# Performance work log

Measured on AMD Instinct MI355X. Metric: run time of the kernel, lower is better.

The kernel has to match this reference:

```python
import jax, jax.numpy as jnp
import numpy as np

NUM_EXPERTS = 16
HIDDEN = 2048
INTERMEDIATE = 1408
TOTAL_TOKENS = 32768  # tokens pre-sorted by expert assignment


def setup_inputs() -> dict:
    key = jax.random.key(0)
    k1, k2, k3, k4 = jax.random.split(key, 4)
    x = jax.random.normal(k1, (TOTAL_TOKENS, HIDDEN), dtype=jnp.float32)
    # normal() initializer per module; scale ~N(0, 0.02) like typical kernel_init
    w_gate = jax.random.normal(k2, (NUM_EXPERTS, HIDDEN, INTERMEDIATE), dtype=jnp.float32) * 0.02
    w_up = jax.random.normal(k3, (NUM_EXPERTS, HIDDEN, INTERMEDIATE), dtype=jnp.float32) * 0.02
    w_down = jax.random.normal(k4, (NUM_EXPERTS, INTERMEDIATE, HIDDEN), dtype=jnp.float32) * 0.02
    # tokens evenly distributed over experts; sums to TOTAL_TOKENS
    group_sizes = jnp.full((NUM_EXPERTS,), TOTAL_TOKENS // NUM_EXPERTS, dtype=jnp.int32)
    return {"x": x, "w_gate": w_gate, "w_up": w_up, "w_down": w_down,
            "group_sizes": group_sizes}


def reference(x, w_gate, w_up, w_down, group_sizes):
    # Grouped (ragged) GEMMs: rows of x are grouped contiguously by expert,
    # group_sizes[e] rows use expert e's kernel. lax.ragged_dot is the
    # idiomatic grouped-GEMM primitive (no dense [T,E] masking).
    gate = jax.lax.ragged_dot(x, w_gate, group_sizes)      # [T, I]
    up = jax.lax.ragged_dot(x, w_up, group_sizes)          # [T, I]
    h = jax.nn.silu(gate) * up                             # fused SwiGLU gating
    out = jax.lax.ragged_dot(h, w_down, group_sizes)       # [T, H]
    return out
```

## Files before the change

kernel.cpp:

```cpp
#include <hip/hip_runtime.h>
#include <hip/hip_bf16.h>

#define TOKENS 32768
#define NEXP   16
#define HID    2048
#define IMD    1408
#define BM 256
#define BK 64

typedef __bf16 bf16x8 __attribute__((ext_vector_type(8)));
typedef float  f32x4  __attribute__((ext_vector_type(4)));
typedef unsigned short u16x8 __attribute__((ext_vector_type(8)));

using gptr1_t = const __attribute__((address_space(1))) void*;
using lptr3_t = __attribute__((address_space(3))) void*;

static __device__ __forceinline__ unsigned short f2bf(float f) {
  unsigned int x = __builtin_bit_cast(unsigned int, f);
  x += 0x7fffu + ((x >> 16) & 1u);
  return (unsigned short)(x >> 16);
}
static __device__ __forceinline__ float bf2f(unsigned short u) {
  unsigned int x = ((unsigned int)u) << 16;
  return __builtin_bit_cast(float, x);
}
static __device__ __forceinline__ void gload16(const void* g, void* l) {
  __builtin_amdgcn_global_load_lds((gptr1_t)g, (lptr3_t)l, 16, 0, 0);
}
static __device__ __forceinline__ void vwait(int n) {
  switch (n) {
    case 0:  asm volatile("s_waitcnt vmcnt(0)" ::: "memory"); break;
    case 2:  asm volatile("s_waitcnt vmcnt(2)" ::: "memory"); break;
    default: asm volatile("s_waitcnt vmcnt(6)" ::: "memory"); break;
  }
}

__global__ __launch_bounds__(256)
void convert_kernel(const float* __restrict__ in, unsigned short* __restrict__ out, size_t n)
{
  size_t i = ((size_t)blockIdx.x * blockDim.x + threadIdx.x) * 8;
  if (i >= n) return;
  float4 a = *(const float4*)(in + i);
  float4 b = *(const float4*)(in + i + 4);
  u16x8 o;
  o[0] = f2bf(a.x); o[1] = f2bf(a.y); o[2] = f2bf(a.z); o[3] = f2bf(a.w);
  o[4] = f2bf(b.x); o[5] = f2bf(b.y); o[6] = f2bf(b.z); o[7] = f2bf(b.w);
  *(u16x8*)(out + i) = o;
}

__global__ __launch_bounds__(256)
void transpose_conv_kernel(const float* __restrict__ in, unsigned short* __restrict__ out,
                           int K, int N)
{
  __shared__ float tile[32][33];
  const int e = blockIdx.z;
  const float* ip = in + (size_t)e * K * N;
  unsigned short* op = out + (size_t)e * K * N;
  const int c0 = blockIdx.x * 32, r0 = blockIdx.y * 32;
  const int tx = threadIdx.x, ty = threadIdx.y;
#pragma unroll
  for (int i = 0; i < 4; ++i)
    tile[ty + 8 * i][tx] = ip[(size_t)(r0 + ty + 8 * i) * N + c0 + tx];
  __syncthreads();
#pragma unroll
  for (int i = 0; i < 4; ++i)
    op[(size_t)(c0 + ty + 8 * i) * K + r0 + tx] = f2bf(tile[tx][ty + 8 * i]);
}

template<int MODE>
__global__ __launch_bounds__(512, 2)
void gemm_kernel(const unsigned short* __restrict__ A,
                 const unsigned short* __restrict__ B0,
                 const unsigned short* __restrict__ B1,
                 unsigned short* __restrict__ Hc,
                 float* __restrict__ Cf,
                 const int* __restrict__ gs,
                 int K, int N)
{
  constexpr int NRT = TOKENS / BM;

  __shared__ __align__(16) unsigned short lA[2][256 * 64];
  __shared__ __align__(16) unsigned short lB[2][256 * 64];

  const int nwg = gridDim.x;
  const int q = nwg >> 3;
  const int wgid = (blockIdx.x & 7) * q + (blockIdx.x >> 3);
  const int rt = wgid % NRT;
  const int ct = wgid / NRT;
  const int row0 = rt * BM;

  int e = 0;
  { int a0 = 0;
    for (int i = 0; i < NEXP; ++i) { int s = gs[i]; if (row0 < a0 + s) { e = i; break; } a0 += s; } }

  const unsigned short* Ap = A + (size_t)row0 * K;
  const unsigned short* Bg = B0 + (size_t)e * N * K;
  const unsigned short* Bu = (MODE == 0) ? (B1 + (size_t)e * N * K) : nullptr;

  const int tid  = threadIdx.x;
  const int lane = tid & 63, wave = tid >> 6;
  const int wr = wave >> 2, wc = wave & 3;
  const int fr = lane & 15, fq = lane >> 4;

  const int csw0 = ((0 * 4 + fq) ^ (fr & 7)) * 8;
  const int csw1 = ((1 * 4 + fq) ^ (fr & 7)) * 8;

  const int r8   = lane >> 3;
  const int slog = ((lane & 7) ^ (r8 & 7)) * 8;

  const int nt = K / BK;

  f32x4 acc[8][4] = {};

  auto stage = [&](int chunk, int tt) {
    const int buf = tt & 1;
    const int k0 = tt * BK;
#pragma unroll
    for (int w = 0; w < 2; ++w) {
      if (chunk >= 2) {
        const int mh = chunk - 2;
        unsigned short* ldst = &lA[buf][(mh * 128 + w * 64 + wave * 8) * 64];
        const int grow = w * 128 + mh * 64 + wave * 8 + r8;
        gload16(Ap + (size_t)grow * K + k0 + slog, ldst);
      } else {
        const int h = chunk;
        unsigned short* ldst = &lB[buf][(h * 128 + w * 64 + wave * 8) * 64];
        const int rem = w * 64 + wave * 8 + r8;
        const int wcs = rem >> 5, rr = rem & 31;
        if constexpr (MODE == 0) {
          const int gcol = ct * 128 + (wcs * 2 + h) * 16 + (rr & 15);
          const unsigned short* mb = ((rr >> 4) & 1) ? Bu : Bg;
          gload16(mb + (size_t)gcol * K + k0 + slog, ldst);
        } else {
          const int gcol = ct * 256 + wcs * 64 + h * 32 + rr;
          gload16(Bg + (size_t)gcol * K + k0 + slog, ldst);
        }
      }
    }
  };

  bf16x8 a[4], b[4];
  auto phase = [&](int cur, int mh, int kk, bool readB,
                   int stChunk, int tN, bool doStage, int waitN) {
    const unsigned short* Ab = lA[cur];
    const unsigned short* Bb = lB[cur];
    const int csw = kk ? csw1 : csw0;
#pragma unroll
    for (int mf = 0; mf < 4; ++mf)
      a[mf] = *(const bf16x8*)(Ab + (mh * 128 + wr * 64 + mf * 16 + fr) * 64 + csw);
    if (readB) {
#pragma unroll
      for (int nf = 0; nf < 4; ++nf)
        b[nf] = *(const bf16x8*)(Bb + ((nf >> 1) * 128 + wc * 32 + (nf & 1) * 16 + fr) * 64 + csw);
    }
    if (doStage) stage(stChunk, tN);
    __builtin_amdgcn_s_barrier();
    asm volatile("s_waitcnt lgkmcnt(0)" ::: "memory");
    __builtin_amdgcn_s_setprio(1);
#pragma unroll
    for (int mf = 0; mf < 4; ++mf)
#pragma unroll
      for (int nf = 0; nf < 4; ++nf)
        acc[mh * 4 + mf][nf] =
            __builtin_amdgcn_mfma_f32_16x16x32_bf16(a[mf], b[nf], acc[mh * 4 + mf][nf], 0, 0, 0);
    __builtin_amdgcn_s_setprio(0);
    if (waitN >= 0) vwait(waitN);
    __builtin_amdgcn_s_barrier();
  };

  stage(0, 0); stage(1, 0); stage(2, 0); stage(3, 0);
  vwait(0);
  __builtin_amdgcn_s_barrier();

  for (int t = 0; t < nt; ++t) {
    const int cur = t & 1;
    const bool more = (t + 1 < nt);
    phase(cur, 0, 0, true,  0, t + 1, more, more ? 2 : 0);
    phase(cur, 1, 0, false, 1, t + 1, more, -1);
    phase(cur, 0, 1, true,  2, t + 1, more, -1);
    phase(cur, 1, 1, false, 3, t + 1, more, more ? 2 : -1);
  }

#pragma unroll
  for (int mi = 0; mi < 8; ++mi) {
    const int rowb = row0 + wr * 128 + (mi >> 2) * 64 + (mi & 3) * 16 + fq * 4;
    if constexpr (MODE == 0) {
#pragma unroll
      for (int m2 = 0; m2 < 2; ++m2) {
        const int col = ct * 128 + (wc * 2 + m2) * 16 + fr;
        f32x4 g = acc[mi][2 * m2], u = acc[mi][2 * m2 + 1];
#pragma unroll
        for (int r = 0; r < 4; ++r) {
          float gv = g[r];
          float s = gv / (1.f + __expf(-gv)) * u[r];
          Hc[(size_t)(rowb + r) * N + col] = f2bf(s);
        }
      }
    } else {
#pragma unroll
      for (int nf = 0; nf < 4; ++nf) {
        const int col = ct * 256 + wc * 64 + nf * 16 + fr;
        f32x4 v = acc[mi][nf];
#pragma unroll
        for (int r = 0; r < 4; ++r)
          Cf[(size_t)(rowb + r) * N + col] = v[r];
      }
    }
  }
}

extern "C" void kernel_launch(void* const* d_in, const int* in_sizes, int n_in,
                              void* d_out, int out_size, void* d_ws, size_t ws_size,
                              hipStream_t stream)
{
  const float* x  = (const float*)d_in[0];
  const float* wg = (const float*)d_in[1];
  const float* wu = (const float*)d_in[2];
  const float* wd = (const float*)d_in[3];
  const int*   gs = (const int*)d_in[4];
  float* out = (float*)d_out;

  const size_t SZ_XB = (size_t)TOKENS * HID * 2;
  const size_t SZ_W  = (size_t)NEXP * HID * IMD * 2;
  const size_t SZ_H  = (size_t)TOKENS * IMD * 2;
  if (ws_size < SZ_XB + 2 * SZ_W + SZ_H) return;

  char* ws = (char*)d_ws;
  unsigned short* xb  = (unsigned short*)ws;
  unsigned short* wTg = (unsigned short*)(ws + SZ_XB);
  unsigned short* wTu = (unsigned short*)(ws + SZ_XB + SZ_W);
  unsigned short* h   = (unsigned short*)(ws + SZ_XB + 2 * SZ_W);

  const int cvt_grid = (int)(((size_t)TOKENS * HID) / (256 * 8));
  convert_kernel<<<cvt_grid, 256, 0, stream>>>(x, xb, (size_t)TOKENS * HID);

  transpose_conv_kernel<<<dim3(IMD / 32, HID / 32, NEXP), dim3(32, 8), 0, stream>>>(wg, wTg, HID, IMD);
  transpose_conv_kernel<<<dim3(IMD / 32, HID / 32, NEXP), dim3(32, 8), 0, stream>>>(wu, wTu, HID, IMD);
  gemm_kernel<0><<<(TOKENS / BM) * (IMD / 128), 512, 0, stream>>>(
      xb, wTg, wTu, h, nullptr, gs, HID, IMD);

  transpose_conv_kernel<<<dim3(HID / 32, IMD / 32, NEXP), dim3(32, 8), 0, stream>>>(wd, wTg, IMD, HID);
  gemm_kernel<1><<<(TOKENS / BM) * (HID / 256), 512, 0, stream>>>(
      h, wTg, nullptr, nullptr, out, gs, IMD, HID);
}
```

Measured before the change: 931.1 us.

## Restructure GEMM main loop with double-buffered register fragments and fewer barriers

Replaces the four-phase loop, which had two barriers per phase, with a schedule that keeps two sets of A and B register fragments. LDS reads for the next k-substep are issued before the MFMAs of the current one, so each K tile needs only two barriers. The vmcnt wait points are retuned for this (vwait 4 and 2), and the prologue no longer waits for all loads to finish. This targets barrier stalls and LDS-read latency, at the cost of extra VGPRs and tighter ordering assumptions on async global-to-LDS loads.

```diff
diff --git a/kernel.cpp b/kernel.cpp
--- a/kernel.cpp
+++ b/kernel.cpp
@@ -31,6 +31,7 @@
   switch (n) {
     case 0:  asm volatile("s_waitcnt vmcnt(0)" ::: "memory"); break;
     case 2:  asm volatile("s_waitcnt vmcnt(2)" ::: "memory"); break;
+    case 4:  asm volatile("s_waitcnt vmcnt(4)" ::: "memory"); break;
     default: asm volatile("s_waitcnt vmcnt(6)" ::: "memory"); break;
   }
 }
@@ -70,8 +71,8 @@
 template<int MODE>
 __global__ __launch_bounds__(512, 2)
 void gemm_kernel(const unsigned short* __restrict__ A,
-                 const unsigned short* __restrict__ B0,
-                 const unsigned short* __restrict__ B1,
+                 const unsigned short* __restrict__ B0m,
+                 const unsigned short* __restrict__ B1m,
                  unsigned short* __restrict__ Hc,
                  float* __restrict__ Cf,
                  const int* __restrict__ gs,
@@ -94,8 +95,8 @@
     for (int i = 0; i < NEXP; ++i) { int s = gs[i]; if (row0 < a0 + s) { e = i; break; } a0 += s; } }
 
   const unsigned short* Ap = A + (size_t)row0 * K;
-  const unsigned short* Bg = B0 + (size_t)e * N * K;
-  const unsigned short* Bu = (MODE == 0) ? (B1 + (size_t)e * N * K) : nullptr;
+  const unsigned short* Bg = B0m + (size_t)e * N * K;
+  const unsigned short* Bu = (MODE == 0) ? (B1m + (size_t)e * N * K) : nullptr;
 
   const int tid  = threadIdx.x;
   const int lane = tid & 63, wave = tid >> 6;
@@ -111,6 +112,7 @@
   const int nt = K / BK;
 
   f32x4 acc[8][4] = {};
+  bf16x8 aX[4], aY[4], b0[4], b1[4];
 
   auto stage = [&](int chunk, int tt) {
     const int buf = tt & 1;
@@ -139,46 +141,67 @@
     }
   };
 
-  bf16x8 a[4], b[4];
-  auto phase = [&](int cur, int mh, int kk, bool readB,
-                   int stChunk, int tN, bool doStage, int waitN) {
-    const unsigned short* Ab = lA[cur];
-    const unsigned short* Bb = lB[cur];
+  auto readA = [&](bf16x8* d, const unsigned short* base, int mh, int kk) {
     const int csw = kk ? csw1 : csw0;
 #pragma unroll
     for (int mf = 0; mf < 4; ++mf)
-      a[mf] = *(const bf16x8*)(Ab + (mh * 128 + wr * 64 + mf * 16 + fr) * 64 + csw);
-    if (readB) {
+      d[mf] = *(const bf16x8*)(base + (mh * 128 + wr * 64 + mf * 16 + fr) * 64 + csw);
+  };
+  auto readB = [&](bf16x8* d, const unsigned short* base, int kk) {
+    const int csw = kk ? csw1 : csw0;
+#pragma unroll
+    for (int nf = 0; nf < 4; ++nf)
+      d[nf] = *(const bf16x8*)(base + ((nf >> 1) * 128 + wc * 32 + (nf & 1) * 16 + fr) * 64 + csw);
+  };
+  auto mfma16 = [&](int ab, const bf16x8* a, const bf16x8* b) {
+    __builtin_amdgcn_s_setprio(1);
+#pragma unroll
+    for (int mf = 0; mf < 4; ++mf)
 #pragma unroll
       for (int nf = 0; nf < 4; ++nf)
-        b[nf] = *(const bf16x8*)(Bb + ((nf >> 1) * 128 + wc * 32 + (nf & 1) * 16 + fr) * 64 + csw);
-    }
-    if (doStage) stage(stChunk, tN);
-    __builtin_amdgcn_s_barrier();
-    asm volatile("s_waitcnt lgkmcnt(0)" ::: "memory");
-    __builtin_amdgcn_s_setprio(1);
-#pragma unroll
-    for (int mf = 0; mf < 4; ++mf)
-#pragma unroll
-      for (int nf = 0; nf < 4; ++nf)
-        acc[mh * 4 + mf][nf] =
-            __builtin_amdgcn_mfma_f32_16x16x32_bf16(a[mf], b[nf], acc[mh * 4 + mf][nf], 0, 0, 0);
+        acc[ab + mf][nf] =
+            __builtin_amdgcn_mfma_f32_16x16x32_bf16(a[mf], b[nf], acc[ab + mf][nf], 0, 0, 0);
     __builtin_amdgcn_s_setprio(0);
-    if (waitN >= 0) vwait(waitN);
-    __builtin_amdgcn_s_barrier();
   };
 
   stage(0, 0); stage(1, 0); stage(2, 0); stage(3, 0);
-  vwait(0);
+  vwait(2);
   __builtin_amdgcn_s_barrier();
+  __builtin_amdgcn_sched_barrier(0);
+  readA(aX, lA[0], 0, 0);
+  readB(b0, lB[0], 0);
 
   for (int t = 0; t < nt; ++t) {
     const int cur = t & 1;
     const bool more = (t + 1 < nt);
-    phase(cur, 0, 0, true,  0, t + 1, more, more ? 2 : 0);
-    phase(cur, 1, 0, false, 1, t + 1, more, -1);
-    phase(cur, 0, 1, true,  2, t + 1, more, -1);
-    phase(cur, 1, 1, false, 3, t + 1, more, more ? 2 : -1);
+    const unsigned short* Ab = lA[cur];
+    const unsigned short* Bb = lB[cur];
+
+    readA(aY, Ab, 0, 1);
+    readB(b1, Bb, 1);
+    if (more) stage(0, t + 1);
+    mfma16(0, aX, b0);
+    if (more) stage(1, t + 1);
+    mfma16(0, aY, b1);
+
+    vwait(more ? 4 : 0);
+    __builtin_amdgcn_s_barrier();
+    __builtin_amdgcn_sched_barrier(0);
+
+    readA(aX, Ab, 1, 0);
+    if (more) stage(2, t + 1);
+    mfma16(4, aX, b0);
+    readA(aY, Ab, 1, 1);
+    if (more) stage(3, t + 1);
+    mfma16(4, aY, b1);
+
+    if (more) {
+      vwait(2);
+      __builtin_amdgcn_s_barrier();
+      __builtin_amdgcn_sched_barrier(0);
+      readA(aX, lA[cur ^ 1], 0, 0);
+      readB(b0, lB[cur ^ 1], 0);
+    }
   }
 
 #pragma unroll
```

Measured after the change: 962.3 us. +3.3%, slower.

## Switch GEMM to 32x32x16 MFMA with inline-asm LDS reads and software pipelining

Applied to the files above, without the earlier changes.

Replaces the 16x16x32 MFMA tiling with 32x32x16 bf16 MFMAs on f32x16 accumulators, which changes the LDS layout mapping for the A and B tiles and reduces the number of LDS fragment reads per FLOP. The k-loop is restructured so LDS reads go through inline-asm ds_read_b128 and are software-pipelined across three register sets, with partial lgkmcnt waits. The loop now ends with a single barrier per k-tile instead of several per-phase barriers. K and N become template parameters so loop counts are compile-time constants. Risks include higher register pressure, and correctness now depends on hand-managed waitcnt and the new swizzle layout.

```diff
diff --git a/kernel.cpp b/kernel.cpp
--- a/kernel.cpp
+++ b/kernel.cpp
@@ -10,6 +10,7 @@
 
 typedef __bf16 bf16x8 __attribute__((ext_vector_type(8)));
 typedef float  f32x4  __attribute__((ext_vector_type(4)));
+typedef float  f32x16 __attribute__((ext_vector_type(16)));
 typedef unsigned short u16x8 __attribute__((ext_vector_type(8)));
 
 using gptr1_t = const __attribute__((address_space(1))) void*;
@@ -27,12 +28,19 @@
 static __device__ __forceinline__ void gload16(const void* g, void* l) {
   __builtin_amdgcn_global_load_lds((gptr1_t)g, (lptr3_t)l, 16, 0, 0);
 }
-static __device__ __forceinline__ void vwait(int n) {
-  switch (n) {
-    case 0:  asm volatile("s_waitcnt vmcnt(0)" ::: "memory"); break;
-    case 2:  asm volatile("s_waitcnt vmcnt(2)" ::: "memory"); break;
-    default: asm volatile("s_waitcnt vmcnt(6)" ::: "memory"); break;
-  }
+static __device__ __forceinline__ void vwait0() {
+  asm volatile("s_waitcnt vmcnt(0)" ::: "memory");
+}
+static __device__ __forceinline__ void lgkm6() {
+  asm volatile("s_waitcnt lgkmcnt(6)" ::: "memory");
+}
+static __device__ __forceinline__ void lgkm0() {
+  asm volatile("s_waitcnt lgkmcnt(0)" ::: "memory");
+}
+static __device__ __forceinline__ f32x4 ds128(unsigned addr) {
+  f32x4 d;
+  asm volatile("ds_read_b128 %0, %1" : "=&v"(d) : "v"(addr));
+  return d;
 }
 
 __global__ __launch_bounds__(256)
@@ -67,24 +75,24 @@
     op[(size_t)(c0 + ty + 8 * i) * K + r0 + tx] = f2bf(tile[tx][ty + 8 * i]);
 }
 
-template<int MODE>
+template<int MODE, int K, int N>
 __global__ __launch_bounds__(512, 2)
 void gemm_kernel(const unsigned short* __restrict__ A,
-                 const unsigned short* __restrict__ B0,
-                 const unsigned short* __restrict__ B1,
+                 const unsigned short* __restrict__ B0m,
+                 const unsigned short* __restrict__ B1m,
                  unsigned short* __restrict__ Hc,
                  float* __restrict__ Cf,
-                 const int* __restrict__ gs,
-                 int K, int N)
+                 const int* __restrict__ gs)
 {
   constexpr int NRT = TOKENS / BM;
+  constexpr int nt  = K / BK;
 
   __shared__ __align__(16) unsigned short lA[2][256 * 64];
   __shared__ __align__(16) unsigned short lB[2][256 * 64];
 
   const int nwg = gridDim.x;
-  const int q = nwg >> 3;
-  const int wgid = (blockIdx.x & 7) * q + (blockIdx.x >> 3);
+  const int qq = nwg >> 3;
+  const int wgid = (blockIdx.x & 7) * qq + (blockIdx.x >> 3);
   const int rt = wgid % NRT;
   const int ct = wgid / NRT;
   const int row0 = rt * BM;
@@ -94,23 +102,27 @@
     for (int i = 0; i < NEXP; ++i) { int s = gs[i]; if (row0 < a0 + s) { e = i; break; } a0 += s; } }
 
   const unsigned short* Ap = A + (size_t)row0 * K;
-  const unsigned short* Bg = B0 + (size_t)e * N * K;
-  const unsigned short* Bu = (MODE == 0) ? (B1 + (size_t)e * N * K) : nullptr;
+  const unsigned short* Bg = B0m + (size_t)e * N * K;
+  const unsigned short* Bu = (MODE == 0) ? (B1m + (size_t)e * N * K) : nullptr;
 
   const int tid  = threadIdx.x;
   const int lane = tid & 63, wave = tid >> 6;
   const int wr = wave >> 2, wc = wave & 3;
-  const int fr = lane & 15, fq = lane >> 4;
-
-  const int csw0 = ((0 * 4 + fq) ^ (fr & 7)) * 8;
-  const int csw1 = ((1 * 4 + fq) ^ (fr & 7)) * 8;
-
-  const int r8   = lane >> 3;
-  const int slog = ((lane & 7) ^ (r8 & 7)) * 8;
-
-  const int nt = K / BK;
-
-  f32x4 acc[8][4] = {};
+  const int l31 = lane & 31, hi = lane >> 5, l7 = lane & 7;
+  const int r8 = lane >> 3;
+  const int slog = ((lane & 7) ^ r8) * 8;
+
+  const unsigned sw0 = (unsigned)(((0 + hi) ^ l7) * 16);
+  const unsigned sw1 = (unsigned)(((2 + hi) ^ l7) * 16);
+  const unsigned sw2 = (unsigned)(((4 + hi) ^ l7) * 16);
+  const unsigned sw3 = (unsigned)(((6 + hi) ^ l7) * 16);
+
+  const unsigned lAb = (unsigned)(unsigned long long)(const void*)&lA[0][0];
+  const unsigned lBb = (unsigned)(unsigned long long)(const void*)&lB[0][0];
+  const unsigned aRow = lAb + (unsigned)((wr * 128 + l31) * 128);
+  const unsigned bRow = lBb + (unsigned)((wc * 64 + l31) * 128);
+
+  f32x16 acc[4][2] = {};
 
   auto stage = [&](int chunk, int tt) {
     const int buf = tt & 1;
@@ -118,92 +130,102 @@
 #pragma unroll
     for (int w = 0; w < 2; ++w) {
       if (chunk >= 2) {
-        const int mh = chunk - 2;
-        unsigned short* ldst = &lA[buf][(mh * 128 + w * 64 + wave * 8) * 64];
-        const int grow = w * 128 + mh * 64 + wave * 8 + r8;
+        const int c = chunk - 2;
+        unsigned short* ldst = &lA[buf][(c * 128 + w * 64 + wave * 8) * 64];
+        const int grow = c * 128 + w * 64 + wave * 8 + r8;
         gload16(Ap + (size_t)grow * K + k0 + slog, ldst);
       } else {
-        const int h = chunk;
-        unsigned short* ldst = &lB[buf][(h * 128 + w * 64 + wave * 8) * 64];
+        unsigned short* ldst = &lB[buf][(chunk * 128 + w * 64 + wave * 8) * 64];
         const int rem = w * 64 + wave * 8 + r8;
-        const int wcs = rem >> 5, rr = rem & 31;
+        const int v = chunk * 128 + rem;
         if constexpr (MODE == 0) {
-          const int gcol = ct * 128 + (wcs * 2 + h) * 16 + (rr & 15);
-          const unsigned short* mb = ((rr >> 4) & 1) ? Bu : Bg;
+          const int wcq = v >> 6, p = (v >> 5) & 1, i = v & 31;
+          const unsigned short* mb = p ? Bu : Bg;
+          const int gcol = ct * 128 + wcq * 32 + i;
           gload16(mb + (size_t)gcol * K + k0 + slog, ldst);
         } else {
-          const int gcol = ct * 256 + wcs * 64 + h * 32 + rr;
+          const int gcol = ct * 256 + v;
           gload16(Bg + (size_t)gcol * K + k0 + slog, ldst);
         }
       }
     }
   };
 
-  bf16x8 a[4], b[4];
-  auto phase = [&](int cur, int mh, int kk, bool readB,
-                   int stChunk, int tN, bool doStage, int waitN) {
-    const unsigned short* Ab = lA[cur];
-    const unsigned short* Bb = lB[cur];
-    const int csw = kk ? csw1 : csw0;
-#pragma unroll
-    for (int mf = 0; mf < 4; ++mf)
-      a[mf] = *(const bf16x8*)(Ab + (mh * 128 + wr * 64 + mf * 16 + fr) * 64 + csw);
-    if (readB) {
-#pragma unroll
-      for (int nf = 0; nf < 4; ++nf)
-        b[nf] = *(const bf16x8*)(Bb + ((nf >> 1) * 128 + wc * 32 + (nf & 1) * 16 + fr) * 64 + csw);
-    }
-    if (doStage) stage(stChunk, tN);
+  auto rdA = [&](f32x4* d, unsigned sw, unsigned bufoff) {
+#pragma unroll
+    for (int m = 0; m < 4; ++m)
+      d[m] = ds128(aRow + bufoff + (unsigned)(m * 4096) + sw);
+  };
+  auto rdB = [&](f32x4* d, unsigned sw, unsigned bufoff) {
+    d[0] = ds128(bRow + bufoff + sw);
+    d[1] = ds128(bRow + bufoff + 4096u + sw);
+  };
+  auto cluster = [&](const f32x4* a4, const f32x4* b2) {
+    __builtin_amdgcn_sched_barrier(0);
+    __builtin_amdgcn_s_setprio(1);
+#pragma unroll
+    for (int m = 0; m < 4; ++m)
+#pragma unroll
+      for (int n2 = 0; n2 < 2; ++n2)
+        acc[m][n2] = __builtin_amdgcn_mfma_f32_32x32x16_bf16(
+            __builtin_bit_cast(bf16x8, a4[m]), __builtin_bit_cast(bf16x8, b2[n2]),
+            acc[m][n2], 0, 0, 0);
+    __builtin_amdgcn_s_setprio(0);
+    __builtin_amdgcn_sched_barrier(0);
+  };
+
+  stage(0, 0); stage(1, 0); stage(2, 0); stage(3, 0);
+  vwait0();
+  __builtin_amdgcn_s_barrier();
+
+  f32x4 aS0[4], bS0[2], aS1[4], bS1[2], aS2[4], bS2[2];
+
+  for (int t = 0; t < nt; ++t) {
+    const unsigned bufoff = (unsigned)((t & 1) * 32768);
+    const bool more = (t + 1 < nt);
+
+    rdA(aS0, sw0, bufoff); rdB(bS0, sw0, bufoff);
+    rdA(aS1, sw1, bufoff); rdB(bS1, sw1, bufoff);
+    lgkm6();
+    cluster(aS0, bS0);
+    if (more) { stage(0, t + 1); stage(1, t + 1); }
+    rdA(aS2, sw2, bufoff); rdB(bS2, sw2, bufoff);
+    lgkm6();
+    cluster(aS1, bS1);
+    if (more) { stage(2, t + 1); stage(3, t + 1); }
+    rdA(aS0, sw3, bufoff); rdB(bS0, sw3, bufoff);
+    lgkm6();
+    cluster(aS2, bS2);
+    lgkm0();
+    cluster(aS0, bS0);
+
+    vwait0();
     __builtin_amdgcn_s_barrier();
-    asm volatile("s_waitcnt lgkmcnt(0)" ::: "memory");
-    __builtin_amdgcn_s_setprio(1);
-#pragma unroll
-    for (int mf = 0; mf < 4; ++mf)
-#pragma unroll
-      for (int nf = 0; nf < 4; ++nf)
-        acc[mh * 4 + mf][nf] =
-            __builtin_amdgcn_mfma_f32_16x16x32_bf16(a[mf], b[nf], acc[mh * 4 + mf][nf], 0, 0, 0);
-    __builtin_amdgcn_s_setprio(0);
-    if (waitN >= 0) vwait(waitN);
-    __builtin_amdgcn_s_barrier();
-  };
-
-  stage(0, 0); stage(1, 0); stage(2, 0); stage(3, 0);
-  vwait(0);
-  __builtin_amdgcn_s_barrier();
-
-  for (int t = 0; t < nt; ++t) {
-    const int cur = t & 1;
-    const bool more = (t + 1 < nt);
-    phase(cur, 0, 0, true,  0, t + 1, more, more ? 2 : 0);
-    phase(cur, 1, 0, false, 1, t + 1, more, -1);
-    phase(cur, 0, 1, true,  2, t + 1, more, -1);
-    phase(cur, 1, 1, false, 3, t + 1, more, more ? 2 : -1);
   }
 
 #pragma unroll
-  for (int mi = 0; mi < 8; ++mi) {
-    const int rowb = row0 + wr * 128 + (mi >> 2) * 64 + (mi & 3) * 16 + fq * 4;
+  for (int m = 0; m < 4; ++m) {
+    const int rowb = row0 + wr * 128 + m * 32 + 4 * hi;
     if constexpr (MODE == 0) {
-#pragma unroll
-      for (int m2 = 0; m2 < 2; ++m2) {
-        const int col = ct * 128 + (wc * 2 + m2) * 16 + fr;
-        f32x4 g = acc[mi][2 * m2], u = acc[mi][2 * m2 + 1];
-#pragma unroll
-        for (int r = 0; r < 4; ++r) {
-          float gv = g[r];
-          float s = gv / (1.f + __expf(-gv)) * u[r];
-          Hc[(size_t)(rowb + r) * N + col] = f2bf(s);
-        }
+      const int col = ct * 128 + wc * 32 + l31;
+      f32x16 g = acc[m][0], u = acc[m][1];
+#pragma unroll
+      for (int r = 0; r < 16; ++r) {
+        const int row = rowb + (r & 3) + 8 * (r >> 2);
+        float gv = g[r];
+        float s = gv / (1.f + __expf(-gv)) * u[r];
+        Hc[(size_t)row * N + col] = f2bf(s);
       }
     } else {
 #pragma unroll
-      for (int nf = 0; nf < 4; ++nf) {
-        const int col = ct * 256 + wc * 64 + nf * 16 + fr;
-        f32x4 v = acc[mi][nf];
-#pragma unroll
-        for (int r = 0; r < 4; ++r)
-          Cf[(size_t)(rowb + r) * N + col] = v[r];
+      for (int n2 = 0; n2 < 2; ++n2) {
+        const int col = ct * 256 + wc * 64 + n2 * 32 + l31;
+        f32x16 v = acc[m][n2];
+#pragma unroll
+        for (int r = 0; r < 16; ++r) {
+          const int row = rowb + (r & 3) + 8 * (r >> 2);
+          Cf[(size_t)row * N + col] = v[r];
+        }
       }
     }
   }
@@ -236,10 +258,10 @@
 
   transpose_conv_kernel<<<dim3(IMD / 32, HID / 32, NEXP), dim3(32, 8), 0, stream>>>(wg, wTg, HID, IMD);
   transpose_conv_kernel<<<dim3(IMD / 32, HID / 32, NEXP), dim3(32, 8), 0, stream>>>(wu, wTu, HID, IMD);
-  gemm_kernel<0><<<(TOKENS / BM) * (IMD / 128), 512, 0, stream>>>(
-      xb, wTg, wTu, h, nullptr, gs, HID, IMD);
+  gemm_kernel<0, HID, IMD><<<(TOKENS / BM) * (IMD / 128), 512, 0, stream>>>(
+      xb, wTg, wTu, h, nullptr, gs);
 
   transpose_conv_kernel<<<dim3(HID / 32, IMD / 32, NEXP), dim3(32, 8), 0, stream>>>(wd, wTg, IMD, HID);
-  gemm_kernel<1><<<(TOKENS / BM) * (HID / 256), 512, 0, stream>>>(
-      h, wTg, nullptr, nullptr, out, gs, IMD, HID);
-}
+  gemm_kernel<1, IMD, HID><<<(TOKENS / BM) * (HID / 256), 512, 0, stream>>>(
+      h, wTg, nullptr, nullptr, out, gs);
+}
```

Result: faster. 876.1 us (-5.9%).

## Restructure GEMM main loop into three phases with precomputed load pointers

Applied to the files above, without the earlier changes.

Reworks the GEMM inner loop from four phases per K-tile into three. B fragments are read once per kk half and reused across both M halves, and the tile layout is changed so each wave owns contiguous 128-row A and 64-column B slices. K and N become template constants, and global-load base pointers and LDS destinations are precomputed. The goal is fewer LDS reads and barriers per tile and less address arithmetic. It costs more live registers (two A and two B fragment sets), which may pressure occupancy under the 512x2 launch bounds.

```diff
diff --git a/kernel.cpp b/kernel.cpp
--- a/kernel.cpp
+++ b/kernel.cpp
@@ -33,6 +33,10 @@
     case 2:  asm volatile("s_waitcnt vmcnt(2)" ::: "memory"); break;
     default: asm volatile("s_waitcnt vmcnt(6)" ::: "memory"); break;
   }
+}
+static __device__ __forceinline__ void lg0sb() {
+  asm volatile("s_waitcnt lgkmcnt(0)" ::: "memory");
+  __builtin_amdgcn_sched_barrier(0);
 }
 
 __global__ __launch_bounds__(256)
@@ -67,24 +71,24 @@
     op[(size_t)(c0 + ty + 8 * i) * K + r0 + tx] = f2bf(tile[tx][ty + 8 * i]);
 }
 
-template<int MODE>
+template<int MODE, int K, int N>
 __global__ __launch_bounds__(512, 2)
 void gemm_kernel(const unsigned short* __restrict__ A,
-                 const unsigned short* __restrict__ B0,
-                 const unsigned short* __restrict__ B1,
+                 const unsigned short* __restrict__ B0m,
+                 const unsigned short* __restrict__ B1m,
                  unsigned short* __restrict__ Hc,
                  float* __restrict__ Cf,
-                 const int* __restrict__ gs,
-                 int K, int N)
+                 const int* __restrict__ gs)
 {
   constexpr int NRT = TOKENS / BM;
+  constexpr int nt  = K / BK;
 
   __shared__ __align__(16) unsigned short lA[2][256 * 64];
   __shared__ __align__(16) unsigned short lB[2][256 * 64];
 
   const int nwg = gridDim.x;
-  const int q = nwg >> 3;
-  const int wgid = (blockIdx.x & 7) * q + (blockIdx.x >> 3);
+  const int qq = nwg >> 3;
+  const int wgid = (blockIdx.x & 7) * qq + (blockIdx.x >> 3);
   const int rt = wgid % NRT;
   const int ct = wgid / NRT;
   const int row0 = rt * BM;
@@ -94,116 +98,146 @@
     for (int i = 0; i < NEXP; ++i) { int s = gs[i]; if (row0 < a0 + s) { e = i; break; } a0 += s; } }
 
   const unsigned short* Ap = A + (size_t)row0 * K;
-  const unsigned short* Bg = B0 + (size_t)e * N * K;
-  const unsigned short* Bu = (MODE == 0) ? (B1 + (size_t)e * N * K) : nullptr;
+  const unsigned short* Bg = B0m + (size_t)e * N * K;
+  const unsigned short* Bu = (MODE == 0) ? (B1m + (size_t)e * N * K) : nullptr;
 
   const int tid  = threadIdx.x;
   const int lane = tid & 63, wave = tid >> 6;
   const int wr = wave >> 2, wc = wave & 3;
   const int fr = lane & 15, fq = lane >> 4;
 
-  const int csw0 = ((0 * 4 + fq) ^ (fr & 7)) * 8;
-  const int csw1 = ((1 * 4 + fq) ^ (fr & 7)) * 8;
-
-  const int r8   = lane >> 3;
-  const int slog = ((lane & 7) ^ (r8 & 7)) * 8;
-
-  const int nt = K / BK;
-
-  f32x4 acc[8][4] = {};
-
-  auto stage = [&](int chunk, int tt) {
-    const int buf = tt & 1;
-    const int k0 = tt * BK;
-#pragma unroll
-    for (int w = 0; w < 2; ++w) {
-      if (chunk >= 2) {
-        const int mh = chunk - 2;
-        unsigned short* ldst = &lA[buf][(mh * 128 + w * 64 + wave * 8) * 64];
-        const int grow = w * 128 + mh * 64 + wave * 8 + r8;
-        gload16(Ap + (size_t)grow * K + k0 + slog, ldst);
-      } else {
-        const int h = chunk;
-        unsigned short* ldst = &lB[buf][(h * 128 + w * 64 + wave * 8) * 64];
-        const int rem = w * 64 + wave * 8 + r8;
-        const int wcs = rem >> 5, rr = rem & 31;
-        if constexpr (MODE == 0) {
-          const int gcol = ct * 128 + (wcs * 2 + h) * 16 + (rr & 15);
-          const unsigned short* mb = ((rr >> 4) & 1) ? Bu : Bg;
-          gload16(mb + (size_t)gcol * K + k0 + slog, ldst);
-        } else {
-          const int gcol = ct * 256 + wcs * 64 + h * 32 + rr;
-          gload16(Bg + (size_t)gcol * K + k0 + slog, ldst);
-        }
-      }
-    }
-  };
-
-  bf16x8 a[4], b[4];
-  auto phase = [&](int cur, int mh, int kk, bool readB,
-                   int stChunk, int tN, bool doStage, int waitN) {
-    const unsigned short* Ab = lA[cur];
-    const unsigned short* Bb = lB[cur];
-    const int csw = kk ? csw1 : csw0;
+  const int csw0 = ((0 + fq) ^ (fr & 7)) * 8;
+  const int csw1 = ((4 + fq) ^ (fr & 7)) * 8;
+
+  const int srow = wave * 8 + (lane >> 3);
+  const int slog = ((lane & 7) ^ ((lane >> 3) & 7)) * 8;
+
+  const unsigned short* aCom = Ap + (size_t)srow * K + slog;
+  const unsigned short* bCom;
+  if constexpr (MODE == 0) {
+    const int p = (srow >> 4) & 1;
+    const int colb = ct * 128 + ((srow >> 5) << 4) + (srow & 15);
+    bCom = (p ? Bu : Bg) + (size_t)colb * K + slog;
+  } else {
+    bCom = Bg + (size_t)(ct * 256 + srow) * K + slog;
+  }
+  constexpr size_t BSW = (MODE == 0) ? (size_t)32 * K : (size_t)64 * K;
+
+  const int dA0 = (0   + wave * 8) * 64, dA1 = (128 + wave * 8) * 64;
+  const int dA2 = (64  + wave * 8) * 64, dA3 = (192 + wave * 8) * 64;
+  const int dB0 = (0   + wave * 8) * 64, dB1 = (64  + wave * 8) * 64;
+  const int dB2 = (128 + wave * 8) * 64, dB3 = (192 + wave * 8) * 64;
+
+  f32x4 acc[2][4][4] = {};
+  bf16x8 aT[4], aU[4], b0[4], b1[4];
+
+  auto stC2 = [&](int koff, unsigned short* An) {
+    gload16(aCom + koff, An + dA0);
+    gload16(aCom + (size_t)128 * K + koff, An + dA1);
+  };
+  auto stC3 = [&](int koff, unsigned short* An) {
+    gload16(aCom + (size_t)64 * K + koff, An + dA2);
+    gload16(aCom + (size_t)192 * K + koff, An + dA3);
+  };
+  auto stC0 = [&](int koff, unsigned short* Bn) {
+    gload16(bCom + koff, Bn + dB0);
+    gload16(bCom + BSW + koff, Bn + dB1);
+  };
+  auto stC1 = [&](int koff, unsigned short* Bn) {
+    gload16(bCom + 2 * BSW + koff, Bn + dB2);
+    gload16(bCom + 3 * BSW + koff, Bn + dB3);
+  };
+
+  auto rdA = [&](bf16x8* d, const unsigned short* Ab, int mh, int csw) {
 #pragma unroll
     for (int mf = 0; mf < 4; ++mf)
-      a[mf] = *(const bf16x8*)(Ab + (mh * 128 + wr * 64 + mf * 16 + fr) * 64 + csw);
-    if (readB) {
+      d[mf] = *(const bf16x8*)(Ab + (wr * 128 + mh * 64 + mf * 16 + fr) * 64 + csw);
+  };
+  auto rdB = [&](bf16x8* d, const unsigned short* Bb, int csw) {
+#pragma unroll
+    for (int nf = 0; nf < 4; ++nf)
+      d[nf] = *(const bf16x8*)(Bb + (wc * 64 + nf * 16 + fr) * 64 + csw);
+  };
+  auto MF = [&](int mh, const bf16x8* a, const bf16x8* b) {
+#pragma unroll
+    for (int mf = 0; mf < 4; ++mf)
 #pragma unroll
       for (int nf = 0; nf < 4; ++nf)
-        b[nf] = *(const bf16x8*)(Bb + ((nf >> 1) * 128 + wc * 32 + (nf & 1) * 16 + fr) * 64 + csw);
-    }
-    if (doStage) stage(stChunk, tN);
-    __builtin_amdgcn_s_barrier();
-    asm volatile("s_waitcnt lgkmcnt(0)" ::: "memory");
-    __builtin_amdgcn_s_setprio(1);
-#pragma unroll
-    for (int mf = 0; mf < 4; ++mf)
-#pragma unroll
-      for (int nf = 0; nf < 4; ++nf)
-        acc[mh * 4 + mf][nf] =
-            __builtin_amdgcn_mfma_f32_16x16x32_bf16(a[mf], b[nf], acc[mh * 4 + mf][nf], 0, 0, 0);
-    __builtin_amdgcn_s_setprio(0);
-    if (waitN >= 0) vwait(waitN);
-    __builtin_amdgcn_s_barrier();
-  };
-
-  stage(0, 0); stage(1, 0); stage(2, 0); stage(3, 0);
+        acc[mh][mf][nf] =
+            __builtin_amdgcn_mfma_f32_16x16x32_bf16(a[mf], b[nf], acc[mh][mf][nf], 0, 0, 0);
+  };
+
+  stC2(0, lA[0]); stC0(0, lB[0]); stC1(0, lB[0]); stC3(0, lA[0]);
   vwait(0);
   __builtin_amdgcn_s_barrier();
 
+#pragma unroll 1
   for (int t = 0; t < nt; ++t) {
-    const int cur = t & 1;
+    const unsigned short* Ab = lA[t & 1];
+    const unsigned short* Bb = lB[t & 1];
+    unsigned short* An = lA[(t + 1) & 1];
+    unsigned short* Bn = lB[(t + 1) & 1];
     const bool more = (t + 1 < nt);
-    phase(cur, 0, 0, true,  0, t + 1, more, more ? 2 : 0);
-    phase(cur, 1, 0, false, 1, t + 1, more, -1);
-    phase(cur, 0, 1, true,  2, t + 1, more, -1);
-    phase(cur, 1, 1, false, 3, t + 1, more, more ? 2 : -1);
-  }
-
-#pragma unroll
-  for (int mi = 0; mi < 8; ++mi) {
-    const int rowb = row0 + wr * 128 + (mi >> 2) * 64 + (mi & 3) * 16 + fq * 4;
-    if constexpr (MODE == 0) {
-#pragma unroll
-      for (int m2 = 0; m2 < 2; ++m2) {
-        const int col = ct * 128 + (wc * 2 + m2) * 16 + fr;
-        f32x4 g = acc[mi][2 * m2], u = acc[mi][2 * m2 + 1];
-#pragma unroll
-        for (int r = 0; r < 4; ++r) {
-          float gv = g[r];
-          float s = gv / (1.f + __expf(-gv)) * u[r];
-          Hc[(size_t)(rowb + r) * N + col] = f2bf(s);
+    const int koff = (t + 1) * BK;
+
+    rdA(aT, Ab, 0, csw0); rdB(b0, Bb, csw0);
+    if (more) { stC2(koff, An); stC0(koff, Bn); }
+    __builtin_amdgcn_s_barrier();
+    lg0sb();
+    __builtin_amdgcn_s_setprio(1);
+    MF(0, aT, b0);
+    __builtin_amdgcn_s_setprio(0);
+    __builtin_amdgcn_s_barrier();
+
+    rdA(aU, Ab, 0, csw1); rdB(b1, Bb, csw1);
+    if (more) stC1(koff, Bn);
+    __builtin_amdgcn_s_barrier();
+    lg0sb();
+    __builtin_amdgcn_s_setprio(1);
+    MF(0, aU, b1);
+    __builtin_amdgcn_s_setprio(0);
+    vwait(more ? 6 : 0);
+    __builtin_amdgcn_s_barrier();
+
+    rdA(aT, Ab, 1, csw0); rdA(aU, Ab, 1, csw1);
+    if (more) stC3(koff, An);
+    __builtin_amdgcn_s_barrier();
+    lg0sb();
+    __builtin_amdgcn_s_setprio(1);
+    MF(1, aT, b0);
+    MF(1, aU, b1);
+    __builtin_amdgcn_s_setprio(0);
+    if (more) {
+      vwait(2);
+      __builtin_amdgcn_s_barrier();
+    }
+  }
+
+#pragma unroll
+  for (int mh = 0; mh < 2; ++mh) {
+#pragma unroll
+    for (int mf = 0; mf < 4; ++mf) {
+      const int rowb = row0 + wr * 128 + mh * 64 + mf * 16 + fq * 4;
+      if constexpr (MODE == 0) {
+#pragma unroll
+        for (int m2 = 0; m2 < 2; ++m2) {
+          const int col = ct * 128 + (wc * 2 + m2) * 16 + fr;
+          f32x4 g = acc[mh][mf][2 * m2], u = acc[mh][mf][2 * m2 + 1];
+#pragma unroll
+          for (int r = 0; r < 4; ++r) {
+            float gv = g[r];
+            Hc[(size_t)(rowb + r) * N + col] = f2bf(gv / (1.f + __expf(-gv)) * u[r]);
+          }
         }
-      }
-    } else {
-#pragma unroll
-      for (int nf = 0; nf < 4; ++nf) {
-        const int col = ct * 256 + wc * 64 + nf * 16 + fr;
-        f32x4 v = acc[mi][nf];
-#pragma unroll
-        for (int r = 0; r < 4; ++r)
-          Cf[(size_t)(rowb + r) * N + col] = v[r];
+      } else {
+#pragma unroll
+        for (int nf = 0; nf < 4; ++nf) {
+          const int col = ct * 256 + wc * 64 + nf * 16 + fr;
+          f32x4 v = acc[mh][mf][nf];
+#pragma unroll
+          for (int r = 0; r < 4; ++r)
+            Cf[(size_t)(rowb + r) * N + col] = v[r];
+        }
       }
     }
   }
@@ -236,10 +270,10 @@
 
   transpose_conv_kernel<<<dim3(IMD / 32, HID / 32, NEXP), dim3(32, 8), 0, stream>>>(wg, wTg, HID, IMD);
   transpose_conv_kernel<<<dim3(IMD / 32, HID / 32, NEXP), dim3(32, 8), 0, stream>>>(wu, wTu, HID, IMD);
-  gemm_kernel<0><<<(TOKENS / BM) * (IMD / 128), 512, 0, stream>>>(
-      xb, wTg, wTu, h, nullptr, gs, HID, IMD);
+  gemm_kernel<0, HID, IMD><<<(TOKENS / BM) * (IMD / 128), 512, 0, stream>>>(
+      xb, wTg, wTu, h, nullptr, gs);
 
   transpose_conv_kernel<<<dim3(HID / 32, IMD / 32, NEXP), dim3(32, 8), 0, stream>>>(wd, wTg, IMD, HID);
-  gemm_kernel<1><<<(TOKENS / BM) * (HID / 256), 512, 0, stream>>>(
-      h, wTg, nullptr, nullptr, out, gs, IMD, HID);
-}
+  gemm_kernel<1, IMD, HID><<<(TOKENS / BM) * (HID / 256), 512, 0, stream>>>(
+      h, wTg, nullptr, nullptr, out, gs);
+}
```

Result: faster. 885.2 us (-4.9%).
